# Performance work log

Hardware: AMD Instinct MI355X
Metric: run time of the kernel (lower is better)

Reference implementation:

```python
import jax, jax.numpy as jnp
import numpy as np

B, SP, SH, H = 32, 256, 256, 512
D = 2 * H       # input feature dim (2*hidden_size)
E = H // 2      # per-liner output dim
FD = 4 * H      # fusion linear dim
EPS = 1e-13


def setup_inputs() -> dict:
    key = jax.random.key(0)
    ks = jax.random.split(key, 8)
    s = 0.02
    return dict(
        premise_batch=jax.random.normal(ks[0], (B, SP, D), jnp.float32),
        hypothesis_batch=jax.random.normal(ks[1], (B, SH, D), jnp.float32),
        premise_mask=jax.random.randint(ks[2], (B, SP), 0, 2).astype(jnp.int32),
        hypothesis_mask=jax.random.randint(ks[3], (B, SH), 0, 2).astype(jnp.int32),
        W8=jax.random.normal(ks[4], (8, D, E), jnp.float32) * s,   # liner1..8 weights (in,out)
        B8=jnp.zeros((8, E), jnp.float32),
        Wl=jax.random.normal(ks[5], (8 * E, FD), jnp.float32) * s,  # self.liner
        bl=jnp.zeros((FD,), jnp.float32),
        Wp=jax.random.normal(ks[6], (7 * D, H), jnp.float32) * s,   # self._projection
        bp=jnp.zeros((H,), jnp.float32),
    )


def masked_softmax(logits, mask):
    # ESIM-style: multiply logits by mask, softmax, re-mask, renormalize.
    m = mask[:, None, :]                        # (b,1,kv)
    r = jax.nn.softmax(logits * m, axis=-1) * m
    return r / (r.sum(axis=-1, keepdims=True) + EPS)


def fuse(x, imp_self, imp_inter, W8, B8, Wl, bl):
    # x: (b,s,D); imp_*: (b,s,1). Eight modulated views -> liner1..8 -> concat -> liner+ReLU.
    a1 = imp_self * imp_inter
    a2 = imp_self + imp_inter
    a3 = jnp.maximum(imp_self, imp_inter)
    x1 = x * imp_self
    x2 = x * imp_inter
    mx = jnp.maximum(x1, x2)
    feats = jnp.stack([x * a1, x * a2, x * a3, mx,
                       x * (a1 + 1.0), x * (a2 + 1.0), x * (a3 + 1.0), mx + x], 0)  # (8,b,s,D)
    h = jnp.einsum('kbsd,kde->kbse', feats, W8) + B8[:, None, None, :]              # (8,b,s,E)
    cat = jnp.moveaxis(h, 0, 2).reshape(x.shape[0], x.shape[1], 8 * E)              # concat order 1..8
    return jax.nn.relu(cat @ Wl + bl)           # dropout is identity in eval mode


def reference(premise_batch, hypothesis_batch, premise_mask, hypothesis_mask,
              W8, B8, Wl, bl, Wp, bp):
    pm = premise_mask.astype(jnp.float32)
    hm = hypothesis_mask.astype(jnp.float32)
    scale = 1.0 / jnp.sqrt(jnp.float32(premise_batch.shape[-1]))

    sim = jnp.einsum('bpd,bhd->bph', premise_batch, hypothesis_batch) * scale
    ph = masked_softmax(sim, hm)                               # (b,Sp,Sh)
    hp = masked_softmax(sim.transpose(0, 2, 1), pm)            # (b,Sh,Sp)
    att_p = jnp.einsum('bph,bhd->bpd', ph, hypothesis_batch) * pm[:, :, None]
    att_h = jnp.einsum('bhp,bpd->bhd', hp, premise_batch) * hm[:, :, None]

    sp_attn = jax.nn.softmax(jnp.einsum('bpd,bqd->bpq', premise_batch, premise_batch) * scale, axis=-1)
    sh_attn = jax.nn.softmax(jnp.einsum('bpd,bqd->bpq', hypothesis_batch, hypothesis_batch) * scale, axis=-1)
    self_p = sp_attn @ premise_batch
    self_h = sh_attn @ hypothesis_batch

    imp_p = sp_attn.sum(axis=-2)[..., None]        # (b,Sp,1)
    imp_h = sh_attn.sum(axis=-2)[..., None]        # (b,Sh,1)
    inter_imp_h = ph.sum(axis=-2)[..., None]       # (b,Sh,1)
    inter_imp_p = hp.sum(axis=-2)[..., None]       # (b,Sp,1)

    p_all = fuse(premise_batch, imp_p, inter_imp_p, W8, B8, Wl, bl)
    h_all = fuse(hypothesis_batch, imp_h, inter_imp_h, W8, B8, Wl, bl)

    enh_p = jnp.concatenate([premise_batch, att_p, self_p, p_all,
                             premise_batch * att_p, premise_batch - att_p], axis=-1)
    enh_h = jnp.concatenate([hypothesis_batch, att_h, self_h, h_all,
                             hypothesis_batch * att_h, hypothesis_batch - att_h], axis=-1)
    out_p = jax.nn.relu(enh_p @ Wp + bp)
    out_h = jax.nn.relu(enh_h @ Wp + bp)
    return out_p, out_h
```

## Files before the change

### kernel.cpp

```cpp
#include <hip/hip_runtime.h>
#include <hip/hip_bf16.h>
#include <cmath>

#define BB 32
#define SS 256
#define DD 1024
#define EE 256
#define FDIM 2048
#define HH 512
#define KOUT6 (6 * 1024)
#define NROW (BB * SS)
#define NROW2 (2 * NROW)
#define SIMSZ ((size_t)BB * SS * SS)

static constexpr float SCALE = 1.0f / 32.0f;
static constexpr float EPSF  = 1e-13f;

typedef __attribute__((ext_vector_type(8))) short bf16x8;
typedef __attribute__((ext_vector_type(4))) float f32x4;

__device__ inline float4 ld4(const float* p) { return *(const float4*)p; }
__device__ inline ushort f2b(float f) {
    uint x = __float_as_uint(f);
    x += 0x7fffu + ((x >> 16) & 1u);
    return (ushort)(x >> 16);
}
__device__ inline float b2f(ushort u) { return __uint_as_float(((uint)u) << 16); }
__device__ inline bf16x8 cvt8(const float* v) {
    bf16x8 r;
#pragma unroll
    for (int j = 0; j < 8; ++j) r[j] = (short)f2b(v[j]);
    return r;
}
__device__ inline void b2f8(bf16x8 v, float* o) {
#pragma unroll
    for (int j = 0; j < 8; ++j) o[j] = b2f((ushort)v[j]);
}

typedef __attribute__((address_space(1))) const uchar gas_t;
typedef __attribute__((address_space(3))) uchar las_t;
__device__ inline void gll16(const ushort* g, ushort* l) {
    __builtin_amdgcn_global_load_lds((gas_t*)g, (las_t*)l, 16, 0, 0);
}

__device__ inline int swz_orig_2d() {
    const int n   = blockIdx.y * gridDim.x + blockIdx.x;
    const int tot = gridDim.x * gridDim.y;
    return (n & 7) * (tot >> 3) + (n >> 3);
}
__device__ inline int swz_orig_3d() {
    const int n   = (blockIdx.z * gridDim.y + blockIdx.y) * gridDim.x + blockIdx.x;
    const int tot = gridDim.x * gridDim.y * gridDim.z;
    return (n & 7) * (tot >> 3) + (n >> 3);
}

__global__ __launch_bounds__(256)
void tpose_cvt_k(const float* __restrict__ in, ushort* __restrict__ out,
                 int K, int N, size_t inStride, size_t outStride) {
    __shared__ float T[32][33];
    const float* ib = in  + (size_t)blockIdx.z * inStride;
    ushort*      ob = out + (size_t)blockIdx.z * outStride;
    const int k0 = blockIdx.x * 32, n0 = blockIdx.y * 32;
    const int tx = threadIdx.x & 31, ty = threadIdx.x >> 5;
#pragma unroll
    for (int i = 0; i < 4; ++i) T[ty + 8 * i][tx] = ib[(size_t)(k0 + ty + 8 * i) * N + n0 + tx];
    __syncthreads();
#pragma unroll
    for (int i = 0; i < 4; ++i)
        ob[(size_t)(n0 + ty + 8 * i) * K + k0 + tx] = f2b(T[tx][ty + 8 * i]);
}

__global__ __launch_bounds__(256)
void tpose_wp_k(const float* __restrict__ Wp, ushort* __restrict__ out) {
    __shared__ float T[32][33];
    const int k0 = blockIdx.x * 32, n0 = blockIdx.y * 32;
    const int tx = threadIdx.x & 31, ty = threadIdx.x >> 5;
#pragma unroll
    for (int i = 0; i < 4; ++i) {
        const int k = k0 + ty + 8 * i, n = n0 + tx;
        float v = Wp[(size_t)k * HH + n];
        if (k < DD)           v += Wp[(size_t)(k + 6 * DD) * HH + n];
        else if (k < 2 * DD)  v -= Wp[(size_t)(k + 5 * DD) * HH + n];
        T[ty + 8 * i][tx] = v;
    }
    __syncthreads();
#pragma unroll
    for (int i = 0; i < 4; ++i)
        out[(size_t)(n0 + ty + 8 * i) * KOUT6 + k0 + tx] = f2b(T[tx][ty + 8 * i]);
}

__global__ __launch_bounds__(256)
void cvt_xb_k(const float* __restrict__ P, const float* __restrict__ H,
              ushort* __restrict__ Xb) {
    const int idx = blockIdx.x * 256 + threadIdx.x;
    const int row = idx >> 7, chunk = idx & 127;
    const size_t off = (size_t)row * DD + chunk * 8;
    const float* X = (row < NROW) ? (P + off) : (H + off - (size_t)NROW * DD);
    const float4 x0 = ld4(X), x1 = ld4(X + 4);
    float xv[8] = {x0.x, x0.y, x0.z, x0.w, x1.x, x1.y, x1.z, x1.w};
    *(bf16x8*)&Xb[off] = cvt8(xv);
}

__global__ __launch_bounds__(256)
void prep_xprod_k(const float* __restrict__ P, const float* __restrict__ H,
                  const ushort* __restrict__ attAb,
                  ushort* __restrict__ Xb, ushort* __restrict__ prodb) {
    const int idx = blockIdx.x * 256 + threadIdx.x;
    const int row = idx >> 7, chunk = idx & 127;
    const size_t off = (size_t)row * DD + chunk * 8;
    const float* X = (row < NROW) ? (P + off) : (H + off - (size_t)NROW * DD);
    const float4 x0 = ld4(X), x1 = ld4(X + 4);
    float xv[8] = {x0.x, x0.y, x0.z, x0.w, x1.x, x1.y, x1.z, x1.w};
    float av[8];
    b2f8(*(const bf16x8*)&attAb[off], av);
    float pv[8];
#pragma unroll
    for (int j = 0; j < 8; ++j) pv[j] = xv[j] * av[j];
    *(bf16x8*)&Xb[off]    = cvt8(xv);
    *(bf16x8*)&prodb[off] = cvt8(pv);
}

__global__ __launch_bounds__(256)
void reduce_out_k(float* __restrict__ out, const float* __restrict__ p1,
                  const float* __restrict__ bp) {
    const int gid = blockIdx.x * 256 + threadIdx.x;
    const size_t o = (size_t)gid * 4;
    const float4 a = ld4(&out[o]);
    const float4 b = ld4(&p1[o]);
    const float4 bv = ld4(&bp[(int)(o & 511)]);
    *(float4*)&out[o] = make_float4(fmaxf(a.x + b.x + bv.x, 0.f),
                                    fmaxf(a.y + b.y + bv.y, 0.f),
                                    fmaxf(a.z + b.z + bv.z, 0.f),
                                    fmaxf(a.w + b.w + bv.w, 0.f));
}

__global__ __launch_bounds__(256)
void softmax4_k(ushort* __restrict__ simPH, ushort* __restrict__ simPHT,
                ushort* __restrict__ simPP, ushort* __restrict__ simHH,
                const int* __restrict__ pma, const int* __restrict__ hma) {
    const int job = blockIdx.y;
    ushort* buf = job == 0 ? simPH : job == 1 ? simPHT : job == 2 ? simPP : simHH;
    const int* mask = job == 0 ? hma : job == 1 ? pma : nullptr;
    const int w = threadIdx.x >> 6, lane = threadIdx.x & 63;
    const int row = blockIdx.x * 4 + w;
    const int b = row >> 8;
    ushort* rp = buf + (size_t)row * SS + lane * 4;
    ushort4 u = *(const ushort4*)rp;
    float z[4], mj[4];
    const ushort uv[4] = {u.x, u.y, u.z, u.w};
#pragma unroll
    for (int c = 0; c < 4; ++c) {
        const float v = b2f(uv[c]);
        float m = 1.f;
        if (mask) m = (float)mask[b * SS + lane * 4 + c];
        mj[c] = m; z[c] = v * m;
    }
    float M = fmaxf(fmaxf(z[0], z[1]), fmaxf(z[2], z[3]));
#pragma unroll
    for (int off = 1; off < 64; off <<= 1) M = fmaxf(M, __shfl_xor(M, off));
    float e[4], r[4], sz = 0.f, sr = 0.f;
#pragma unroll
    for (int c = 0; c < 4; ++c) {
        e[c] = expf(z[c] - M);
        r[c] = e[c] * mj[c];
        sz += e[c]; sr += r[c];
    }
#pragma unroll
    for (int off = 1; off < 64; off <<= 1) {
        sz += __shfl_xor(sz, off);
        sr += __shfl_xor(sr, off);
    }
    ushort4 o;
    if (mask) {
        const float d = 1.f / (sr + EPSF * sz);
        o.x = f2b(r[0] * d); o.y = f2b(r[1] * d); o.z = f2b(r[2] * d); o.w = f2b(r[3] * d);
    } else {
        const float d = 1.f / sz;
        o.x = f2b(e[0] * d); o.y = f2b(e[1] * d); o.z = f2b(e[2] * d); o.w = f2b(e[3] * d);
    }
    *(ushort4*)rp = o;
}

__global__ __launch_bounds__(256)
void colsum_p1_k(const ushort* __restrict__ simPP, const ushort* __restrict__ simHH,
                 const ushort* __restrict__ simPHT, const ushort* __restrict__ simPH,
                 float* __restrict__ pbuf) {
    const int job = blockIdx.y, b = blockIdx.x, rc = blockIdx.z, j = threadIdx.x;
    const ushort* src = job == 0 ? simPP : job == 1 ? simHH : job == 2 ? simPHT : simPH;
    const ushort* Mb = src + (size_t)b * SS * SS + (size_t)rc * 32 * SS;
    float s = 0.f;
#pragma unroll 4
    for (int i = 0; i < 32; ++i) s += b2f(Mb[i * SS + j]);
    pbuf[(((size_t)job * BB + b) * 8 + rc) * SS + j] = s;
}

__global__ __launch_bounds__(256)
void colsum_p2_k(const float* __restrict__ pbuf,
                 float* __restrict__ impS, float* __restrict__ impI) {
    const int job = blockIdx.y, b = blockIdx.x, j = threadIdx.x;
    const float* pb = pbuf + ((size_t)job * BB + b) * 8 * SS;
    float s = 0.f;
#pragma unroll
    for (int rc = 0; rc < 8; ++rc) s += pb[rc * SS + j];
    float* dst = job == 0 ? impS : job == 1 ? impS + NROW : job == 2 ? impI : impI + NROW;
    dst[b * SS + j] = s;
}

#define LSWZ(kg, r) ((r) ^ ((kg) << 1))
#define SIG(r) (((r) >> 1) & 3)
#define FRAG_R(T, r) (*(const bf16x8*)T[kq][LSWZ(kg_dummy_, r)])
#undef FRAG_R
#define FRAG_R(T, r) (*(const bf16x8*)T[kq][LSWZ(kq, r)])
#define FRAG_G(T, r) (*(const bf16x8*)&T[r][(kq ^ SIG(r)) * 8])
#define FRAG_G64(T, r, kh) (*(const bf16x8*)&T[r][((((kh) << 2) + kq) ^ ((r) & 7)) * 8])

#define MFMA_TAIL(afr, bfr, ac)                                                      \
    _Pragma("unroll") for (int m = 0; m < 4; ++m)                                    \
        _Pragma("unroll") for (int n = 0; n < 4; ++n)                                \
            ac[m][n] = __builtin_amdgcn_mfma_f32_16x16x32_bf16(                      \
                afr[m], bfr[n], ac[m][n], 0, 0, 0);

#define MFMA_CORE_G64()                                                              \
    _Pragma("unroll") for (int kh_ = 0; kh_ < 2; ++kh_) {                            \
        bf16x8 afr[4], bfr[4];                                                       \
        _Pragma("unroll") for (int m = 0; m < 4; ++m)                                \
            afr[m] = FRAG_G64(As, wr + m * 16 + fr, kh_);                            \
        _Pragma("unroll") for (int n = 0; n < 4; ++n)                                \
            bfr[n] = FRAG_G64(Bs, wc + n * 16 + fr, kh_);                            \
        MFMA_TAIL(afr, bfr, acc)                                                     \
    }

#define MFMA_CORE_DB(AT, BT_)                                                        \
    {                                                                                \
        bf16x8 afr[4], bfr[4];                                                       \
        _Pragma("unroll") for (int m = 0; m < 4; ++m) afr[m] = FRAG_G(AT, wr + m * 16 + fr); \
        _Pragma("unroll") for (int n = 0; n < 4; ++n) bfr[n] = FRAG_G(BT_, wc + n * 16 + fr); \
        MFMA_TAIL(afr, bfr, acc)                                                     \
    }

#define MFMA_PREAMBLE()                                                              \
    const int tid = threadIdx.x;                                                     \
    const int lane = tid & 63;                                                       \
    const int w = tid >> 6;                                                          \
    const int wr = (w >> 1) * 64, wc = (w & 1) * 64;                                 \
    const int fr = lane & 15;                                                        \
    const int kq = lane >> 4;                                                        \
    const int rq = kq * 4;                                                           \
    f32x4 acc[4][4] = {};

#define GLL_STAGE2(seg, pitch, r0, kloc, T)                                          \
    {                                                                                \
        const int rl0_ = w * 32 + (lane >> 2);                                       \
        const int cp_ = lane & 3;                                                    \
        gll16((seg) + (size_t)((r0) + rl0_) * (pitch) + (kloc) + ((cp_ ^ SIG(rl0_)) * 8), \
              &T[w * 32][0]);                                                        \
        const int rl1_ = rl0_ + 16;                                                  \
        gll16((seg) + (size_t)((r0) + rl1_) * (pitch) + (kloc) + ((cp_ ^ SIG(rl1_)) * 8), \
              &T[w * 32 + 16][0]);                                                   \
    }

#define GLL_STAGE64(seg, pitch, r0, kloc, T)                                         \
    {                                                                                \
        _Pragma("unroll")                                                            \
        for (int ii_ = 0; ii_ < 4; ++ii_) {                                          \
            const int rl_ = w * 32 + ii_ * 8 + (lane >> 3);                          \
            const int cp_ = lane & 7;                                                \
            gll16((seg) + (size_t)((r0) + rl_) * (pitch) + (kloc) + (((cp_ ^ (rl_ & 7))) * 8), \
                  &T[w * 32 + ii_ * 8][0]);                                          \
        }                                                                            \
    }

#define PIPE_WAIT_N()  { asm volatile("s_waitcnt vmcnt(4)" ::: "memory"); __builtin_amdgcn_s_barrier(); }
#define PIPE_WAIT_0()  { asm volatile("s_waitcnt vmcnt(0)" ::: "memory"); __builtin_amdgcn_s_barrier(); }
#define PIPE_POST()    { asm volatile("" ::: "memory"); __builtin_amdgcn_s_barrier(); }

__global__ __launch_bounds__(256)
void mfma_nt_k(const ushort* __restrict__ XbE,
               ushort* __restrict__ simPH, ushort* __restrict__ simPHT,
               ushort* __restrict__ simPP, ushort* __restrict__ simHH) {
    __shared__ __align__(16) ushort As[128][64];
    __shared__ __align__(16) ushort Bs[128][64];
    int orig = swz_orig_3d();
    const int cb = orig & 1; orig >>= 1;
    const int rb = orig & 1; orig >>= 1;
    const int g = orig >> 5, b = orig & 31;
    const ushort* Au = XbE + ((size_t)((g == 2) ? NROW : 0) + (size_t)b * SS) * DD;
    const ushort* Bu = XbE + ((size_t)((g == 1) ? 0 : NROW) + (size_t)b * SS) * DD;
    const int col0 = cb * 128, row0 = rb * 128;
    MFMA_PREAMBLE();
    for (int k0 = 0; k0 < DD; k0 += 64) {
        __syncthreads();
        GLL_STAGE64(Au, DD, row0, k0, As);
        GLL_STAGE64(Bu, DD, col0, k0, Bs);
        __syncthreads();
        MFMA_CORE_G64();
    }
    ushort* Cb = (g == 0 ? simPH : g == 1 ? simPP : simHH) + (size_t)b * SS * SS;
#pragma unroll
    for (int m = 0; m < 4; ++m)
#pragma unroll
        for (int n = 0; n < 4; ++n) {
            const int c = col0 + wc + n * 16 + fr;
            const int r0 = row0 + wr + m * 16 + rq;
#pragma unroll
            for (int r = 0; r < 4; ++r) Cb[(size_t)(r0 + r) * SS + c] = f2b(acc[m][n][r] * SCALE);
            if (g == 0) {
                ushort* Tb = simPHT + (size_t)b * SS * SS;
                ushort4 t;
                t.x = f2b(acc[m][n][0] * SCALE); t.y = f2b(acc[m][n][1] * SCALE);
                t.z = f2b(acc[m][n][2] * SCALE); t.w = f2b(acc[m][n][3] * SCALE);
                *(ushort4*)&Tb[(size_t)c * SS + r0] = t;
            }
        }
}

__global__ __launch_bounds__(256)
void mfma_att_k(const ushort* __restrict__ ph, const ushort* __restrict__ hp,
                const ushort* __restrict__ spA, const ushort* __restrict__ shA,
                const ushort* __restrict__ PbT, const ushort* __restrict__ HbT,
                const int* __restrict__ pma, const int* __restrict__ hma,
                ushort* __restrict__ attAb, ushort* __restrict__ selfAb) {
    __shared__ __align__(16) ushort As[128][64];
    __shared__ __align__(16) ushort Bs[128][64];
    int orig = swz_orig_3d();
    const int x = orig & 7; orig >>= 3;
    const int y = orig & 1; orig >>= 1;
    const int g = orig >> 5, b = orig & 31;
    const ushort* W  = (g == 0 ? ph : g == 1 ? hp : g == 2 ? spA : shA) + (size_t)b * SS * SS;
    const ushort* BT = ((g == 0 || g == 3) ? HbT : PbT) + (size_t)b * DD * SS;
    const int* rmask = g == 0 ? pma + b * SS : g == 1 ? hma + b * SS : nullptr;
    const int side = (g == 1 || g == 3);
    ushort* Ob = (g < 2 ? attAb : selfAb) + ((size_t)side * NROW + (size_t)b * SS) * DD;
    const int col0 = x * 128, row0 = y * 128;
    MFMA_PREAMBLE();
    for (int k0 = 0; k0 < SS; k0 += 64) {
        __syncthreads();
        GLL_STAGE64(W,  SS, row0, k0, As);
        GLL_STAGE64(BT, SS, col0, k0, Bs);
        __syncthreads();
        MFMA_CORE_G64();
    }
#pragma unroll
    for (int m = 0; m < 4; ++m)
#pragma unroll
        for (int n = 0; n < 4; ++n) {
            const int c = col0 + wc + n * 16 + fr;
#pragma unroll
            for (int r = 0; r < 4; ++r) {
                const int rr = row0 + wr + m * 16 + rq + r;
                const float mm = rmask ? (float)rmask[rr] : 1.0f;
                Ob[(size_t)rr * DD + c] = f2b(acc[m][n][r] * mm);
            }
        }
}

__global__ __launch_bounds__(256)
void mfma_fuse_pure_k(const ushort* __restrict__ Xb, const float* __restrict__ impS,
                      const float* __restrict__ impI, const ushort* __restrict__ W8T,
                      const float* __restrict__ B8v, ushort* __restrict__ catb) {
    __shared__ __align__(16) ushort As[2][128][32];
    __shared__ __align__(16) ushort Bs[2][128][32];
    const int orig = swz_orig_2d();
    const int cb = orig % 12, rb = orig / 12;
    const int kidx = cb >> 1;
    const int kf = kidx + (kidx >= 3 ? 1 : 0);
    const int e0 = (cb & 1) * 128, row0 = rb * 128;
    MFMA_PREAMBLE();
    const ushort* Wk = W8T + (size_t)kf * EE * DD;
    GLL_STAGE2(Xb, DD, row0, 0, As[0]);
    GLL_STAGE2(Wk, DD, e0, 0, Bs[0]);
    int cur = 0;
    for (int t = 0; t < DD / 32; ++t) {
        if (t + 1 < DD / 32) {
            GLL_STAGE2(Xb, DD, row0, (t + 1) * 32, As[cur ^ 1]);
            GLL_STAGE2(Wk, DD, e0, (t + 1) * 32, Bs[cur ^ 1]);
            PIPE_WAIT_N();
        } else {
            PIPE_WAIT_0();
        }
        MFMA_CORE_DB(As[cur], Bs[cur]);
        PIPE_POST();
        cur ^= 1;
    }
#pragma unroll
    for (int m = 0; m < 4; ++m)
#pragma unroll
        for (int n = 0; n < 4; ++n) {
            const int el = e0 + wc + n * 16 + fr;
            const float bv = B8v[kf * EE + el];
#pragma unroll
            for (int r = 0; r < 4; ++r) {
                const int row = row0 + wr + m * 16 + rq + r;
                const float s_ = impS[row], i_ = impI[row];
                float coef;
                switch (kf) {
                    case 0: coef = s_ * i_;             break;
                    case 1: coef = s_ + i_;             break;
                    case 2: coef = fmaxf(s_, i_);       break;
                    case 4: coef = s_ * i_ + 1.f;       break;
                    case 5: coef = s_ + i_ + 1.f;       break;
                    default: coef = fmaxf(s_, i_) + 1.f; break;
                }
                catb[(size_t)row * FDIM + kf * EE + el] = f2b(coef * acc[m][n][r] + bv);
            }
        }
}

__global__ __launch_bounds__(256)
void mfma_fuse_dual_k(const ushort* __restrict__ Xb, const float* __restrict__ impS,
                      const float* __restrict__ impI, const ushort* __restrict__ W8T,
                      const float* __restrict__ B8v, ushort* __restrict__ catb) {
    __shared__ __align__(16) ushort AsX[4][128][8];
    __shared__ __align__(16) ushort AsP[4][128][8];
    __shared__ __align__(16) ushort Bs[128][32];
    const int orig = swz_orig_2d();
    const int cb = orig & 3, rb = orig >> 2;
    const int kf = (cb >> 1) ? 7 : 3;
    const int e0 = (cb & 1) * 128, row0 = rb * 128;
    MFMA_PREAMBLE();
    f32x4 accP[4][4] = {};
    const ushort* Wk = W8T + (size_t)kf * EE * DD;
    for (int k0 = 0; k0 < DD; k0 += 32) {
        bf16x8 xr[2], pr[2];
#pragma unroll
        for (int i = 0; i < 2; ++i) {
            const int cid = tid + i * 256, srow = cid >> 2, skc = (cid & 3) * 8;
            xr[i] = *(const bf16x8*)&Xb[(size_t)(row0 + srow) * DD + k0 + skc];
#pragma unroll
            for (int j = 0; j < 8; ++j) {
                const short s = xr[i][j];
                pr[i][j] = (s & (short)0x8000) ? (short)0 : s;
            }
        }
        __syncthreads();
        GLL_STAGE2(Wk, DD, e0, k0, Bs);
#pragma unroll
        for (int i = 0; i < 2; ++i) {
            const int cid = tid + i * 256, kg = cid & 3, rr = LSWZ(kg, cid >> 2);
            *(bf16x8*)AsX[kg][rr] = xr[i];
            *(bf16x8*)AsP[kg][rr] = pr[i];
        }
        __syncthreads();
        {
            bf16x8 ax[4], ap[4], bfr[4];
#pragma unroll
            for (int m = 0; m < 4; ++m) {
                ax[m] = FRAG_R(AsX, wr + m * 16 + fr);
                ap[m] = FRAG_R(AsP, wr + m * 16 + fr);
            }
#pragma unroll
            for (int n = 0; n < 4; ++n) bfr[n] = FRAG_G(Bs, wc + n * 16 + fr);
            MFMA_TAIL(ax, bfr, acc)
            MFMA_TAIL(ap, bfr, accP)
        }
    }
#pragma unroll
    for (int m = 0; m < 4; ++m)
#pragma unroll
        for (int n = 0; n < 4; ++n) {
            const int el = e0 + wc + n * 16 + fr;
            const float bv = B8v[kf * EE + el];
#pragma unroll
            for (int r = 0; r < 4; ++r) {
                const int row = row0 + wr + m * 16 + rq + r;
                const float s_ = impS[row], i_ = impI[row];
                const float smax = fmaxf(s_, i_), smin = fminf(s_, i_);
                const float gg = (kf == 3) ? smin : smin + 1.f;
                catb[(size_t)row * FDIM + kf * EE + el] =
                    f2b((smax - smin) * accP[m][n][r] + gg * acc[m][n][r] + bv);
            }
        }
}

__global__ __launch_bounds__(256)
void mfma_lin_k(const ushort* __restrict__ A, const ushort* __restrict__ BT,
                const float* __restrict__ bias, ushort* __restrict__ C) {
    __shared__ __align__(16) ushort As[2][128][32];
    __shared__ __align__(16) ushort Bs[2][128][32];
    const int orig = swz_orig_2d();
    const int col0 = (orig & 15) * 128, row0 = (orig >> 4) * 128;
    MFMA_PREAMBLE();
    GLL_STAGE2(A,  FDIM, row0, 0, As[0]);
    GLL_STAGE2(BT, FDIM, col0, 0, Bs[0]);
    int cur = 0;
    for (int t = 0; t < FDIM / 32; ++t) {
        if (t + 1 < FDIM / 32) {
            GLL_STAGE2(A,  FDIM, row0, (t + 1) * 32, As[cur ^ 1]);
            GLL_STAGE2(BT, FDIM, col0, (t + 1) * 32, Bs[cur ^ 1]);
            PIPE_WAIT_N();
        } else {
            PIPE_WAIT_0();
        }
        MFMA_CORE_DB(As[cur], Bs[cur]);
        PIPE_POST();
        cur ^= 1;
    }
#pragma unroll
    for (int m = 0; m < 4; ++m)
#pragma unroll
        for (int n = 0; n < 4; ++n) {
            const int c = col0 + wc + n * 16 + fr;
            const float bv = bias[c];
#pragma unroll
            for (int r = 0; r < 4; ++r) {
                const int rr = row0 + wr + m * 16 + rq + r;
                C[(size_t)rr * FDIM + c] = f2b(fmaxf(acc[m][n][r] + bv, 0.f));
            }
        }
}

__device__ inline void out_seg(int k0, const ushort* Xb, const ushort* attAb,
                               const ushort* selfAb, const ushort* pallb,
                               const ushort* prodb,
                               const ushort*& seg, int& pitch, int& kloc) {
    switch (k0 >> 10) {
        case 0:  seg = Xb;     pitch = DD;   kloc = k0;          break;
        case 1:  seg = attAb;  pitch = DD;   kloc = k0 - DD;     break;
        case 2:  seg = selfAb; pitch = DD;   kloc = k0 - 2 * DD; break;
        case 3:
        case 4:  seg = pallb;  pitch = FDIM; kloc = k0 - 3 * DD; break;
        default: seg = prodb;  pitch = DD;   kloc = k0 - 5 * DD; break;
    }
}

__global__ __launch_bounds__(256)
void mfma_out_k(const ushort* __restrict__ Xb, const ushort* __restrict__ attAb,
                const ushort* __restrict__ selfAb, const ushort* __restrict__ pallb,
                const ushort* __restrict__ prodb, const ushort* __restrict__ WpT,
                const float* __restrict__ bp, float* __restrict__ dst0,
                float* __restrict__ dst1, int kchunk, int finalize) {
    __shared__ __align__(16) ushort As[2][128][32];
    __shared__ __align__(16) ushort Bs[2][128][32];
    int orig = swz_orig_3d();
    const int x = orig & 3; orig >>= 2;
    const int y = orig & 127; orig >>= 7;
    const int z = orig;
    const int col0 = x * 128, row0 = y * 128;
    const int kbase = z * kchunk;
    float* dst = z == 0 ? dst0 : dst1;
    MFMA_PREAMBLE();
    {
        const ushort* seg; int pitch, kloc;
        out_seg(kbase, Xb, attAb, selfAb, pallb, prodb, seg, pitch, kloc);
        GLL_STAGE2(seg, pitch, row0, kloc, As[0]);
        GLL_STAGE2(WpT, KOUT6, col0, kbase, Bs[0]);
    }
    int cur = 0;
    const int NT = kchunk / 32;
    for (int t = 0; t < NT; ++t) {
        if (t + 1 < NT) {
            const int k0 = kbase + (t + 1) * 32;
            const ushort* seg; int pitch, kloc;
            out_seg(k0, Xb, attAb, selfAb, pallb, prodb, seg, pitch, kloc);
            GLL_STAGE2(seg, pitch, row0, kloc, As[cur ^ 1]);
            GLL_STAGE2(WpT, KOUT6, col0, k0, Bs[cur ^ 1]);
            PIPE_WAIT_N();
        } else {
            PIPE_WAIT_0();
        }
        MFMA_CORE_DB(As[cur], Bs[cur]);
        PIPE_POST();
        cur ^= 1;
    }
#pragma unroll
    for (int m = 0; m < 4; ++m)
#pragma unroll
        for (int n = 0; n < 4; ++n) {
            const int c = col0 + wc + n * 16 + fr;
            const float bv = finalize ? bp[c] : 0.f;
#pragma unroll
            for (int r = 0; r < 4; ++r) {
                const int rr = row0 + wr + m * 16 + rq + r;
                const float v = acc[m][n][r] + bv;
                dst[(size_t)rr * HH + c] = finalize ? fmaxf(v, 0.f) : v;
            }
        }
}

extern "C" void kernel_launch(void* const* d_in, const int* in_sizes, int n_in,
                              void* d_out, int out_size, void* d_ws, size_t ws_size,
                              hipStream_t stream) {
    const float* P   = (const float*)d_in[0];
    const float* Hb  = (const float*)d_in[1];
    const int*   pma = (const int*)d_in[2];
    const int*   hma = (const int*)d_in[3];
    const float* W8  = (const float*)d_in[4];
    const float* B8v = (const float*)d_in[5];
    const float* Wl  = (const float*)d_in[6];
    const float* bl  = (const float*)d_in[7];
    const float* Wp  = (const float*)d_in[8];
    const float* bp  = (const float*)d_in[9];

    char* base = (char*)d_ws;
    ushort* simPH  = (ushort*)base;
    ushort* simPHT = simPH  + SIMSZ;
    ushort* simPP  = simPHT + SIMSZ;
    ushort* simHH  = simPP  + SIMSZ;
    ushort* PbT    = simHH + SIMSZ;
    ushort* HbT    = PbT + (size_t)NROW * DD;
    ushort* catb   = (ushort*)base;
    ushort* Xb     = (ushort*)base;
    ushort* prodb  = Xb + (size_t)NROW2 * DD;
    char* cur = base + (size_t)NROW2 * FDIM * 2;
    auto alloc_f = [&](size_t n) { float*  p = (float*)cur;  cur += n * 4; return p; };
    auto alloc_u = [&](size_t n) { ushort* p = (ushort*)cur; cur += n * 2; return p; };
    float*  impS   = alloc_f(NROW2);
    float*  impI   = alloc_f(NROW2);
    ushort* attAb  = alloc_u((size_t)NROW2 * DD);
    ushort* selfAb = alloc_u((size_t)NROW2 * DD);
    ushort* pallb  = alloc_u((size_t)NROW2 * FDIM);
    ushort* WlT    = alloc_u((size_t)FDIM * FDIM);
    ushort* WpT    = alloc_u((size_t)HH * KOUT6);
    ushort* W8T    = alloc_u((size_t)8 * EE * DD);
    float*  pbuf   = alloc_f((size_t)4 * BB * 8 * SS);
    float*  part1  = alloc_f((size_t)NROW2 * HH);

    ushort* XbE = pallb;

    const size_t need_split = (size_t)((char*)(part1 + (size_t)NROW2 * HH) - base);
    const bool split = ws_size >= need_split;

    float* outp = (float*)d_out;
    const dim3 blk(256);

    cvt_xb_k<<<dim3(NROW2 * DD / 8 / 256), blk, 0, stream>>>(P, Hb, XbE);
    tpose_cvt_k<<<dim3(8, 32, BB), blk, 0, stream>>>(P,  PbT, SS, DD, (size_t)SS * DD, (size_t)DD * SS);
    tpose_cvt_k<<<dim3(8, 32, BB), blk, 0, stream>>>(Hb, HbT, SS, DD, (size_t)SS * DD, (size_t)DD * SS);
    tpose_cvt_k<<<dim3(FDIM / 32, FDIM / 32, 1), blk, 0, stream>>>(Wl, WlT, FDIM, FDIM, 0, 0);
    tpose_wp_k<<<dim3(KOUT6 / 32, HH / 32, 1), blk, 0, stream>>>(Wp, WpT);
    tpose_cvt_k<<<dim3(DD / 32, EE / 32, 8), blk, 0, stream>>>(W8, W8T, DD, EE,
                                                               (size_t)DD * EE, (size_t)EE * DD);

    mfma_nt_k<<<dim3(2, 2, 96), blk, 0, stream>>>(XbE, simPH, simPHT, simPP, simHH);
    softmax4_k<<<dim3(NROW / 4, 4), blk, 0, stream>>>(simPH, simPHT, simPP, simHH, pma, hma);
    colsum_p1_k<<<dim3(BB, 4, 8), blk, 0, stream>>>(simPP, simHH, simPHT, simPH, pbuf);
    colsum_p2_k<<<dim3(BB, 4), blk, 0, stream>>>(pbuf, impS, impI);
    mfma_att_k<<<dim3(8, 2, 128), blk, 0, stream>>>(simPH, simPHT, simPP, simHH, PbT, HbT,
                                                    pma, hma, attAb, selfAb);

    mfma_fuse_pure_k<<<dim3(12, 128), blk, 0, stream>>>(XbE, impS, impI, W8T, B8v, catb);
    mfma_fuse_dual_k<<<dim3(4, 128), blk, 0, stream>>>(XbE, impS, impI, W8T, B8v, catb);
    mfma_lin_k<<<dim3(16, 128), blk, 0, stream>>>(catb, WlT, bl, pallb);
    prep_xprod_k<<<dim3(NROW2 * DD / 8 / 256), blk, 0, stream>>>(P, Hb, attAb, Xb, prodb);
    if (split) {
        mfma_out_k<<<dim3(4, 128, 2), blk, 0, stream>>>(Xb, attAb, selfAb, pallb, prodb,
                                                        WpT, bp, outp, part1, KOUT6 / 2, 0);
        reduce_out_k<<<dim3(NROW2 * HH / 4 / 256), blk, 0, stream>>>(outp, part1, bp);
    } else {
        mfma_out_k<<<dim3(4, 128, 1), blk, 0, stream>>>(Xb, attAb, selfAb, pallb, prodb,
                                                        WpT, bp, outp, outp, KOUT6, 1);
    }

    (void)in_sizes; (void)n_in; (void)out_size; (void)ws_size;
}
```

Measured before the change: 725.8 us.

## Fuse bf16 conversion with transposes and simplify GEMM pipeline barriers

```diff
diff --git a/kernel.cpp b/kernel.cpp
--- a/kernel.cpp
+++ b/kernel.cpp
@@ -90,15 +90,28 @@
 }
 
 __global__ __launch_bounds__(256)
-void cvt_xb_k(const float* __restrict__ P, const float* __restrict__ H,
-              ushort* __restrict__ Xb) {
-    const int idx = blockIdx.x * 256 + threadIdx.x;
-    const int row = idx >> 7, chunk = idx & 127;
-    const size_t off = (size_t)row * DD + chunk * 8;
-    const float* X = (row < NROW) ? (P + off) : (H + off - (size_t)NROW * DD);
-    const float4 x0 = ld4(X), x1 = ld4(X + 4);
-    float xv[8] = {x0.x, x0.y, x0.z, x0.w, x1.x, x1.y, x1.z, x1.w};
-    *(bf16x8*)&Xb[off] = cvt8(xv);
+void prep_xt_k(const float* __restrict__ P, const float* __restrict__ H,
+               ushort* __restrict__ XbE, ushort* __restrict__ PbT,
+               ushort* __restrict__ HbT) {
+    __shared__ float T[32][33];
+    const int z = blockIdx.z;
+    const int side = z >> 5, b = z & 31;
+    const float* in = (side ? H : P) + (size_t)b * SS * DD;
+    ushort* xe = XbE + ((size_t)side * NROW + (size_t)b * SS) * DD;
+    ushort* xt = (side ? HbT : PbT) + (size_t)b * DD * SS;
+    const int d0 = blockIdx.x * 32, s0 = blockIdx.y * 32;
+    const int tx = threadIdx.x & 31, ty = threadIdx.x >> 5;
+#pragma unroll
+    for (int i = 0; i < 4; ++i) {
+        const int s = s0 + ty + 8 * i;
+        const float v = in[(size_t)s * DD + d0 + tx];
+        T[ty + 8 * i][tx] = v;
+        xe[(size_t)s * DD + d0 + tx] = f2b(v);
+    }
+    __syncthreads();
+#pragma unroll
+    for (int i = 0; i < 4; ++i)
+        xt[(size_t)(d0 + ty + 8 * i) * SS + s0 + tx] = f2b(T[tx][ty + 8 * i]);
 }
 
 __global__ __launch_bounds__(256)
@@ -208,8 +221,6 @@
 
 #define LSWZ(kg, r) ((r) ^ ((kg) << 1))
 #define SIG(r) (((r) >> 1) & 3)
-#define FRAG_R(T, r) (*(const bf16x8*)T[kq][LSWZ(kg_dummy_, r)])
-#undef FRAG_R
 #define FRAG_R(T, r) (*(const bf16x8*)T[kq][LSWZ(kq, r)])
 #define FRAG_G(T, r) (*(const bf16x8*)&T[r][(kq ^ SIG(r)) * 8])
 #define FRAG_G64(T, r, kh) (*(const bf16x8*)&T[r][((((kh) << 2) + kq) ^ ((r) & 7)) * 8])
@@ -269,10 +280,6 @@
                   &T[w * 32 + ii_ * 8][0]);                                          \
         }                                                                            \
     }
-
-#define PIPE_WAIT_N()  { asm volatile("s_waitcnt vmcnt(4)" ::: "memory"); __builtin_amdgcn_s_barrier(); }
-#define PIPE_WAIT_0()  { asm volatile("s_waitcnt vmcnt(0)" ::: "memory"); __builtin_amdgcn_s_barrier(); }
-#define PIPE_POST()    { asm volatile("" ::: "memory"); __builtin_amdgcn_s_barrier(); }
 
 __global__ __launch_bounds__(256)
 void mfma_nt_k(const ushort* __restrict__ XbE,
@@ -369,17 +376,15 @@
     const ushort* Wk = W8T + (size_t)kf * EE * DD;
     GLL_STAGE2(Xb, DD, row0, 0, As[0]);
     GLL_STAGE2(Wk, DD, e0, 0, Bs[0]);
+    __syncthreads();
     int cur = 0;
     for (int t = 0; t < DD / 32; ++t) {
         if (t + 1 < DD / 32) {
             GLL_STAGE2(Xb, DD, row0, (t + 1) * 32, As[cur ^ 1]);
             GLL_STAGE2(Wk, DD, e0, (t + 1) * 32, Bs[cur ^ 1]);
-            PIPE_WAIT_N();
-        } else {
-            PIPE_WAIT_0();
         }
         MFMA_CORE_DB(As[cur], Bs[cur]);
-        PIPE_POST();
+        __syncthreads();
         cur ^= 1;
     }
 #pragma unroll
@@ -482,17 +487,15 @@
     MFMA_PREAMBLE();
     GLL_STAGE2(A,  FDIM, row0, 0, As[0]);
     GLL_STAGE2(BT, FDIM, col0, 0, Bs[0]);
+    __syncthreads();
     int cur = 0;
     for (int t = 0; t < FDIM / 32; ++t) {
         if (t + 1 < FDIM / 32) {
             GLL_STAGE2(A,  FDIM, row0, (t + 1) * 32, As[cur ^ 1]);
             GLL_STAGE2(BT, FDIM, col0, (t + 1) * 32, Bs[cur ^ 1]);
-            PIPE_WAIT_N();
-        } else {
-            PIPE_WAIT_0();
         }
         MFMA_CORE_DB(As[cur], Bs[cur]);
-        PIPE_POST();
+        __syncthreads();
         cur ^= 1;
     }
 #pragma unroll
@@ -545,6 +548,7 @@
         GLL_STAGE2(seg, pitch, row0, kloc, As[0]);
         GLL_STAGE2(WpT, KOUT6, col0, kbase, Bs[0]);
     }
+    __syncthreads();
     int cur = 0;
     const int NT = kchunk / 32;
     for (int t = 0; t < NT; ++t) {
@@ -554,12 +558,9 @@
             out_seg(k0, Xb, attAb, selfAb, pallb, prodb, seg, pitch, kloc);
             GLL_STAGE2(seg, pitch, row0, kloc, As[cur ^ 1]);
             GLL_STAGE2(WpT, KOUT6, col0, k0, Bs[cur ^ 1]);
-            PIPE_WAIT_N();
-        } else {
-            PIPE_WAIT_0();
         }
         MFMA_CORE_DB(As[cur], Bs[cur]);
-        PIPE_POST();
+        __syncthreads();
         cur ^= 1;
     }
 #pragma unroll
@@ -623,9 +624,7 @@
     float* outp = (float*)d_out;
     const dim3 blk(256);
 
-    cvt_xb_k<<<dim3(NROW2 * DD / 8 / 256), blk, 0, stream>>>(P, Hb, XbE);
-    tpose_cvt_k<<<dim3(8, 32, BB), blk, 0, stream>>>(P,  PbT, SS, DD, (size_t)SS * DD, (size_t)DD * SS);
-    tpose_cvt_k<<<dim3(8, 32, BB), blk, 0, stream>>>(Hb, HbT, SS, DD, (size_t)SS * DD, (size_t)DD * SS);
+    prep_xt_k<<<dim3(DD / 32, SS / 32, 2 * BB), blk, 0, stream>>>(P, Hb, XbE, PbT, HbT);
     tpose_cvt_k<<<dim3(FDIM / 32, FDIM / 32, 1), blk, 0, stream>>>(Wl, WlT, FDIM, FDIM, 0, 0);
     tpose_wp_k<<<dim3(KOUT6 / 32, HH / 32, 1), blk, 0, stream>>>(Wp, WpT);
     tpose_cvt_k<<<dim3(DD / 32, EE / 32, 8), blk, 0, stream>>>(W8, W8T, DD, EE,
```

Measured after the change: 719.3 us. About the same (-0.9%).
